# Optimization experiments

Measured on AMD Instinct MI355X. Metric: run time of the kernel, lower is better.

## Reference

```python
import jax, jax.numpy as jnp
import numpy as np

EPS = 1e-5
GROUPS = 8


def conv2d(x, w, b, pad):
    y = jax.lax.conv_general_dilated(
        x, w, window_strides=(1, 1), padding=[(pad, pad), (pad, pad)],
        dimension_numbers=('NCHW', 'OIHW', 'NCHW'))
    return y + b[None, :, None, None]


def setup_inputs() -> dict:
    key = jax.random.key(0)
    ks = jax.random.split(key, 8)
    b, c, h, w = 32, 256, 56, 56
    cg = c // GROUPS
    x = jax.random.normal(ks[0], (b, c, h, w), dtype=jnp.float32)
    w1 = jax.random.normal(ks[1], (cg, cg, 1, 1), dtype=jnp.float32) * 0.05
    b1 = jnp.zeros((cg,), dtype=jnp.float32)
    w3a = jax.random.normal(ks[2], (cg, cg, 3, 3), dtype=jnp.float32) * 0.05
    b3a = jnp.zeros((cg,), dtype=jnp.float32)
    w3b = jax.random.normal(ks[3], (c, c, 3, 3), dtype=jnp.float32) * 0.02
    b3b = jnp.zeros((c,), dtype=jnp.float32)
    gn_w = jnp.ones((cg,), dtype=jnp.float32)
    gn_b = jnp.zeros((cg,), dtype=jnp.float32)
    return {"x": x, "w1": w1, "b1": b1, "w3a": w3a, "b3a": b3a,
            "w3b": w3b, "b3b": b3b, "gn_w": gn_w, "gn_b": gn_b}


def reference(x, w1, b1, w3a, b3a, w3b, b3b, gn_w, gn_b):
    b, c, h, w = x.shape
    cg = c // GROUPS
    bg = b * GROUPS
    gx = x.reshape(bg, cg, h, w)

    # spatial attention on grouped channels
    x_h = gx.mean(axis=3, keepdims=True)                       # [bg,cg,h,1]
    x_w = gx.mean(axis=2, keepdims=True).transpose(0, 1, 3, 2)  # [bg,cg,w,1]
    hw = conv2d(jnp.concatenate([x_h, x_w], axis=2), w1, b1, 0)
    xh, xw = hw[:, :, :h], hw[:, :, h:]
    x0 = gx * jax.nn.sigmoid(xh) * jax.nn.sigmoid(xw.transpose(0, 1, 3, 2))

    # GroupNorm with num_groups == num_channels (per-channel over HxW)
    mu = x0.mean(axis=(2, 3), keepdims=True)
    var = x0.var(axis=(2, 3), keepdims=True)
    x1 = (x0 - mu) / jnp.sqrt(var + EPS) * gn_w[None, :, None, None] + gn_b[None, :, None, None]

    x2 = conv2d(gx, w3a, b3a, 1)

    # channel softmax-matmul attention (per group)
    x11 = jax.nn.softmax(x1.mean(axis=(2, 3)), axis=-1)[:, None, :]  # [bg,1,cg]
    x12 = x1.reshape(bg, cg, h * w)
    x21 = jax.nn.softmax(x2.mean(axis=(2, 3)), axis=-1)[:, None, :]
    x22 = x2.reshape(bg, cg, h * w)
    weights1 = (jnp.matmul(x11, x22) + jnp.matmul(x21, x12)).reshape(bg, 1, h, w)

    # BatchNorm2d(affine=False), batch statistics (training mode)
    xr = x0.reshape(b, c, h, w)
    bm = xr.mean(axis=(0, 2, 3), keepdims=True)
    bv = xr.var(axis=(0, 2, 3), keepdims=True)
    x3 = (xr - bm) / jnp.sqrt(bv + EPS)

    x4 = conv2d(x, w3b, b3b, 1)

    # spatial softmax-matmul attention over full channels
    x31 = jax.nn.softmax(x3.mean(axis=1).reshape(b, 1, h * w), axis=-1)  # [b,1,hw]
    x32 = x3.reshape(b, c, h * w).transpose(0, 2, 1)                     # [b,hw,c]
    x41 = jax.nn.softmax(x4.mean(axis=1).reshape(b, 1, h * w), axis=-1)
    x42 = x4.reshape(b, c, h * w).transpose(0, 2, 1)
    weights2 = (jnp.matmul(x31, x42) + jnp.matmul(x41, x32)).reshape(b, c, 1, 1)

    return (gx * jax.nn.sigmoid(weights1)).reshape(b, c, h, w) + x * jax.nn.sigmoid(weights2)
```

## Files before the change

kernel.cpp:

```cpp
#include <hip/hip_runtime.h>
#include <math.h>

#define B  32
#define C  256
#define HH 56
#define WW 56
#define HW 3136
#define G  8
#define CG 32
#define BG 256
#define GC 8192
#define EPSF 1e-5f

typedef __attribute__((ext_vector_type(8))) short short8;
typedef __attribute__((ext_vector_type(4))) float f32x4;

#define GLOAD16(g, l) __builtin_amdgcn_global_load_lds( \
    (const __attribute__((address_space(1))) void*)(g), \
    (__attribute__((address_space(3))) void*)(l), 16, 0, 0)

__device__ __forceinline__ float sigmoidf_(float v){ return 1.0f/(1.0f+__expf(-v)); }
__device__ __forceinline__ unsigned short f2bf(float v){
  unsigned u = __builtin_bit_cast(unsigned, v);
  u = u + 0x7FFFu + ((u>>16)&1u);
  return (unsigned short)(u>>16);
}
__device__ __forceinline__ float bf2f(unsigned short v){
  return __builtin_bit_cast(float, ((unsigned)v)<<16);
}

__global__ void kxt(const float* __restrict__ x, unsigned short* __restrict__ xt){
  int bid = blockIdx.x;
  int b = bid / 196; int r2 = bid % 196; int icb = r2 / 49; int pxb = r2 % 49;
  __shared__ float t[64][65];
  int tid = threadIdx.x;
  #pragma unroll
  for(int k=0;k<16;k++){
    int e = k*256 + tid;
    int ic = e>>6, px = e&63;
    t[ic][px] = x[((size_t)(b*256 + icb*64 + ic))*HW + pxb*64 + px];
  }
  __syncthreads();
  #pragma unroll
  for(int k=0;k<16;k++){
    int e = k*256 + tid;
    int px = e>>6, ic = e&63;
    int pxg = pxb*64 + px;
    int pi = pxg/56, pj = pxg%56;
    xt[(((size_t)b*58 + pi + 1)*58 + pj + 1)*256 + icb*64 + ic] = f2bf(t[ic][px]);
  }
}

__global__ void khalo(unsigned short* __restrict__ xt){
  int bid = blockIdx.x;
  int b = bid/228, hp = bid%228;
  int pi, pj;
  if(hp<58){pi=0;pj=hp;}
  else if(hp<116){pi=57;pj=hp-58;}
  else if(hp<172){pi=hp-116+1;pj=0;}
  else {pi=hp-172+1;pj=57;}
  xt[(((size_t)b*58+pi)*58+pj)*256 + threadIdx.x] = 0;
}

__global__ __launch_bounds__(256) void k1t(const unsigned short* __restrict__ xt,
    float* __restrict__ rowm, float* __restrict__ colm){
  int bid = blockIdx.x;
  int b = bid / 112; int r = bid % 112; int rc = r / 56; int idx = r % 56;
  int c = threadIdx.x;
  const unsigned short* xb = xt + (size_t)b*58*58*256 + c;
  float s = 0.f;
  if(rc == 0){
    #pragma unroll 8
    for(int j=0;j<56;j++) s += bf2f(xb[((size_t)(idx+1)*58 + (j+1))*256]);
    rowm[((size_t)b*256 + c)*56 + idx] = s*(1.0f/56.0f);
  } else {
    #pragma unroll 8
    for(int i=0;i<56;i++) s += bf2f(xb[((size_t)(i+1)*58 + (idx+1))*256]);
    colm[((size_t)b*256 + c)*56 + idx] = s*(1.0f/56.0f);
  }
}

__global__ void k2_hw(const float* __restrict__ rowm, const float* __restrict__ colm,
                      const float* __restrict__ w1, const float* __restrict__ b1,
                      float* __restrict__ sh, float* __restrict__ sw,
                      float* __restrict__ shT, float* __restrict__ swT){
  int bg = blockIdx.x;
  int b = bg>>3, g = bg&7;
  __shared__ float inb[32][112];
  __shared__ float wt[32*32];
  __shared__ float bb[32];
  for(int idx=threadIdx.x; idx<32*56; idx+=blockDim.x){
    int ic=idx/56, p=idx%56;
    inb[ic][p]    = rowm[(bg*32+ic)*56+p];
    inb[ic][56+p] = colm[(bg*32+ic)*56+p];
  }
  for(int idx=threadIdx.x; idx<1024; idx+=blockDim.x) wt[idx]=w1[idx];
  if(threadIdx.x<32) bb[threadIdx.x]=b1[threadIdx.x];
  __syncthreads();
  for(int o=threadIdx.x; o<32*112; o+=blockDim.x){
    int oc=o/112, p=o%112;
    float s=bb[oc];
    #pragma unroll
    for(int ic=0;ic<32;ic++) s += wt[oc*32+ic]*inb[ic][p];
    float sg = sigmoidf_(s);
    int c = g*32+oc;
    if(p<56){
      sh[(bg*32+oc)*56+p]=sg;
      shT[((size_t)b*56+p)*256 + c]=sg;
    } else {
      sw[(bg*32+oc)*56+(p-56)]=sg;
      swT[((size_t)b*56+(p-56))*256 + c]=sg;
    }
  }
}

__global__ void k2b_x11(const float* __restrict__ gnb, const float* __restrict__ b3a, float* __restrict__ x11){
  __shared__ float v[32];
  if(threadIdx.x<32) v[threadIdx.x]=gnb[threadIdx.x];
  __syncthreads();
  if(threadIdx.x==0){
    float m=-1e30f; for(int i=0;i<32;i++) m=fmaxf(m,v[i]);
    float s=0.f; for(int i=0;i<32;i++){ v[i]=__expf(v[i]-m); s+=v[i]; }
    float d=0.f;
    for(int i=0;i<32;i++){ float p=v[i]/s; x11[i]=p; d+=p*b3a[i]; }
    x11[32]=d;
  }
}

__global__ __launch_bounds__(256) void k3t(const unsigned short* __restrict__ xt,
    const float* __restrict__ shT, const float* __restrict__ swT,
    float* __restrict__ gsum, float* __restrict__ gsq){
  int bid = blockIdx.x;
  int b = bid / 56, i = bid % 56;
  int c = threadIdx.x;
  float shv = shT[((size_t)b*56+i)*256 + c];
  const unsigned short* xb = xt + ((size_t)(b*58 + i+1)*58 + 1)*256 + c;
  const float* swp = swT + (size_t)b*56*256 + c;
  float s=0.f, s2=0.f;
  #pragma unroll 8
  for(int j=0;j<56;j++){
    float x0 = bf2f(xb[(size_t)j*256]) * shv * swp[(size_t)j*256];
    s += x0; s2 += x0*x0;
  }
  atomicAdd(&gsum[b*256+c], s);
  atomicAdd(&gsq[b*256+c], s2);
}

__global__ void k4a(const float* __restrict__ gsum, const float* __restrict__ gsq,
                    float* __restrict__ mu, float* __restrict__ istd){
  int gc=blockIdx.x*256+threadIdx.x;
  float m=gsum[gc]*(1.0f/HW);
  float v=gsq[gc]*(1.0f/HW)-m*m;
  mu[gc]=m; istd[gc]=rsqrtf(v+EPSF);
}

__global__ void k4b(const float* __restrict__ gsum, const float* __restrict__ gsq,
                    float* __restrict__ bm, float* __restrict__ binv){
  int c=threadIdx.x;
  float s=0.f,s2=0.f;
  for(int b=0;b<B;b++){ s+=gsum[b*256+c]; s2+=gsq[b*256+c]; }
  float m=s*(1.0f/(B*HW));
  float v=s2*(1.0f/(B*HW))-m*m;
  bm[c]=m; binv[c]=rsqrtf(v+EPSF);
}

__global__ __launch_bounds__(128) void k5m(const unsigned short* __restrict__ xt,
    const unsigned short* __restrict__ wta, const float* __restrict__ x11,
    float* __restrict__ w1a, float* __restrict__ cs2){
  __shared__ short Bs[6*58*32];
  int bid = blockIdx.x;
  int xcd = bid & 7; int idx = bid >> 3;
  int b = xcd + 8*(idx/112); int idx2 = idx % 112;
  int g = idx2 / 14; int pt = idx2 % 14;
  int bg = b*8 + g;
  int i0 = pt*4;
  int tid = threadIdx.x;
  int lane = tid & 63, wv = tid >> 6;
  int q = lane >> 4, rl = lane & 15;
  const unsigned short* xb = xt + (size_t)b*58*58*256 + g*32;

  #pragma unroll
  for(int issue=0; issue<11; ++issue){
    int idxl = issue*128 + tid;
    if(idxl < 1392){
      int pl = idxl >> 2, ch = idxl & 3;
      int r = pl / 58, jj = pl - r*58;
      const unsigned short* src = xb + ((size_t)(i0 + r)*58 + jj)*256 + ((ch ^ ((pl>>1)&3))<<3);
      GLOAD16(src, &Bs[idxl*8]);
    }
  }
  __syncthreads();

  f32x4 acc[2][7];
  #pragma unroll
  for(int mi=0;mi<2;mi++)
    #pragma unroll
    for(int ni=0;ni<7;ni++) acc[mi][ni]=(f32x4){0.f,0.f,0.f,0.f};

  int pr[7], pj[7];
  #pragma unroll
  for(int ni=0;ni<7;ni++){
    int px = wv*112 + ni*16 + rl;
    pr[ni] = px/56; pj[ni] = px - pr[ni]*56;
  }

  for(int tap=0; tap<9; ++tap){
    int dy = tap/3, dx = tap - dy*3;
    short8 a[2], bfr[7];
    #pragma unroll
    for(int mi=0;mi<2;mi++)
      a[mi] = *(const short8*)(wta + tap*1024 + (mi*16+rl)*32 + q*8);
    #pragma unroll
    for(int ni=0;ni<7;ni++){
      int pix = (pr[ni] + dy)*58 + pj[ni] + dx;
      int cs = q ^ ((pix>>1)&3);
      bfr[ni] = *(const short8*)&Bs[pix*32 + cs*8];
    }
    #pragma unroll
    for(int mi=0;mi<2;mi++)
      #pragma unroll
      for(int ni=0;ni<7;ni++)
        acc[mi][ni] = __builtin_amdgcn_mfma_f32_16x16x32_bf16(a[mi], bfr[ni], acc[mi][ni], 0,0,0);
  }

  float x11v[2][4];
  #pragma unroll
  for(int mi=0;mi<2;mi++)
    #pragma unroll
    for(int r=0;r<4;r++) x11v[mi][r] = x11[mi*16 + q*4 + r];
  float x11b = x11[32];
  size_t pxg0 = (size_t)bg*HW + i0*56 + wv*112;
  #pragma unroll
  for(int ni=0;ni<7;ni++){
    float s=0.f;
    #pragma unroll
    for(int mi=0;mi<2;mi++)
      #pragma unroll
      for(int r=0;r<4;r++) s += x11v[mi][r]*acc[mi][ni][r];
    s += __shfl_xor(s,16,64);
    s += __shfl_xor(s,32,64);
    if(lane<16) w1a[pxg0 + ni*16 + lane] = s + x11b;
  }
  #pragma unroll
  for(int mi=0;mi<2;mi++){
    #pragma unroll
    for(int r=0;r<4;r++){
      float s=0.f;
      #pragma unroll
      for(int ni=0;ni<7;ni++) s += acc[mi][ni][r];
      s += __shfl_xor(s,1,64);
      s += __shfl_xor(s,2,64);
      s += __shfl_xor(s,4,64);
      s += __shfl_xor(s,8,64);
      if(rl==0) atomicAdd(&cs2[bg*32 + mi*16 + q*4 + r], s);
    }
  }
}

__global__ void k6(const float* __restrict__ cs2, const float* __restrict__ b3a,
                   const float* __restrict__ mu, const float* __restrict__ istd,
                   const float* __restrict__ gnw, const float* __restrict__ gnb,
                   float* __restrict__ av, float* __restrict__ cst){
  int bg=blockIdx.x; int t=threadIdx.x;
  float m = cs2[bg*32+t]*(1.0f/HW) + b3a[t];
  float mx=m;
  for(int off=16;off>0;off>>=1) mx=fmaxf(mx,__shfl_xor(mx,off,32));
  float e=__expf(m-mx);
  float s=e;
  for(int off=16;off>0;off>>=1) s+=__shfl_xor(s,off,32);
  float x21=e/s;
  int gc=bg*32+t;
  float is=istd[gc];
  av[gc]=x21*is*gnw[t];
  float cv=x21*(gnb[t]-mu[gc]*is*gnw[t]);
  for(int off=16;off>0;off>>=1) cv+=__shfl_xor(cv,off,32);
  if(t==0) cst[bg]=cv;
}

__global__ __launch_bounds__(256) void k7x(const unsigned short* __restrict__ xt,
    const float* __restrict__ shT, const float* __restrict__ swT,
    const float* __restrict__ av, const float* __restrict__ binv, const float* __restrict__ cst,
    const float* __restrict__ w1a, float* __restrict__ sg1, float* __restrict__ s3pre){
  int bid = blockIdx.x; int b = bid/56, i = bid%56;
  __shared__ float shs[256], avs[256], bins[256], cst8[8];
  int tid = threadIdx.x;
  shs[tid]  = shT[((size_t)b*56+i)*256 + tid];
  avs[tid]  = av[b*256 + tid];
  bins[tid] = binv[tid];
  if(tid<8) cst8[tid] = cst[b*8+tid];
  __syncthreads();
  int h = tid>>5, l = tid&31;
  int bg = l>>2;
  int c0 = l*8;
  float sh8[8], av8[8], bi8[8];
  #pragma unroll
  for(int m=0;m<8;m++){ sh8[m]=shs[c0+m]; av8[m]=avs[c0+m]; bi8[m]=bins[c0+m]; }
  float cstv = cst8[bg];
  for(int pass=0; pass<7; ++pass){
    int j = pass*8 + h;
    short8 xv = *(const short8*)(xt + (((size_t)b*58 + i+1)*58 + j+1)*256 + c0);
    const float* swp = swT + ((size_t)b*56 + j)*256 + c0;
    float ws=0.f, s3=0.f;
    #pragma unroll
    for(int m=0;m<8;m++){
      float x0 = bf2f((unsigned short)xv[m]) * sh8[m] * swp[m];
      ws += av8[m]*x0;
      s3 += bi8[m]*x0;
    }
    ws += __shfl_xor(ws,1,64);
    ws += __shfl_xor(ws,2,64);
    s3 += __shfl_xor(s3,1,64);
    s3 += __shfl_xor(s3,2,64);
    s3 += __shfl_xor(s3,4,64);
    s3 += __shfl_xor(s3,8,64);
    s3 += __shfl_xor(s3,16,64);
    int p = i*56 + j;
    if((l&3)==0){
      size_t o = ((size_t)(b*8+bg))*HW + p;
      sg1[o] = sigmoidf_(w1a[o] + ws + cstv);
    }
    if(l==0) s3pre[(size_t)b*HW + p] = s3*(1.0f/256.0f);
  }
}

__global__ void k_softmax_hw(const float* __restrict__ in, float* __restrict__ out, float scale){
  int b=blockIdx.x;
  const float* ip=in+(size_t)b*HW;
  float mx=-1e30f;
  for(int p=threadIdx.x;p<HW;p+=blockDim.x) mx=fmaxf(mx,ip[p]*scale);
  for(int off=32;off>0;off>>=1) mx=fmaxf(mx,__shfl_xor(mx,off,64));
  __shared__ float red[8];
  int wid=threadIdx.x>>6, lane=threadIdx.x&63;
  if(lane==0) red[wid]=mx;
  __syncthreads();
  mx=red[0];
  #pragma unroll
  for(int w=1;w<8;w++) mx=fmaxf(mx,red[w]);
  float s=0.f;
  for(int p=threadIdx.x;p<HW;p+=blockDim.x) s+=__expf(ip[p]*scale-mx);
  for(int off=32;off>0;off>>=1) s+=__shfl_down(s,off,64);
  __shared__ float red2[8];
  if(lane==0) red2[wid]=s;
  __syncthreads();
  s=red2[0];
  #pragma unroll
  for(int w=1;w<8;w++) s+=red2[w];
  float inv=1.0f/s;
  for(int p=threadIdx.x;p<HW;p+=blockDim.x) out[(size_t)b*HW+p]=__expf(ip[p]*scale-mx)*inv;
}

__global__ void kwt(const float* __restrict__ w3b, unsigned short* __restrict__ wt){
  int idx = blockIdx.x*256 + threadIdx.x;
  int tap = idx >> 16; int r = idx & 65535; int oc = r >> 8; int ic = r & 255;
  wt[idx] = f2bf(w3b[((size_t)oc*256 + ic)*9 + tap]);
}

__global__ void kwta(const float* __restrict__ w3a, unsigned short* __restrict__ wta){
  int idx = blockIdx.x*256 + threadIdx.x;
  if(idx < 9216){
    int tap = idx >> 10; int r = idx & 1023; int oc = r >> 5; int ic = r & 31;
    wta[idx] = f2bf(w3a[((size_t)oc*32 + ic)*9 + tap]);
  }
}

__global__ __launch_bounds__(512) void k9m(const unsigned short* __restrict__ xt,
    const unsigned short* __restrict__ wt, const float* __restrict__ x31,
    float* __restrict__ s4pre, float* __restrict__ w2a){
  __shared__ short Ab[2][128*32];
  __shared__ short Bb[2][224*32];
  int bid = blockIdx.x;
  int xcd = bid & 7; int idx = bid >> 3;
  int b = xcd + 8*(idx/28); int rr = idx % 28;
  int pt = rr >> 1; int oct = rr & 1;
  int i0 = pt*4; int ocb = oct*128;
  int tid = threadIdx.x;
  int lane = tid & 63, wv = tid >> 6;
  int wm = wv & 3, wn = wv >> 2;
  int q = lane >> 4, rl = lane & 15;
  const unsigned short* xb = xt + (size_t)b*58*58*256;

  #define STAGE_A(BUF, TAP, IC0) do{ \
    int idxl = tid; int oc_ = idxl>>2, cs_ = idxl&3; \
    const unsigned short* src = wt + (((size_t)(TAP)*256 + ocb + oc_)*256 + (IC0) + (((cs_ ^ ((oc_>>1)&3)))<<3)); \
    GLOAD16(src, &Ab[BUF][idxl*8]); }while(0)
  #define STAGE_B(BUF, TAP, IC0) do{ \
    int dy_ = (TAP)/3, dx_ = (TAP)%3; \
    { int idxl = tid; int px_ = idxl>>2, cs_ = idxl&3; int r_ = px_/56, j_ = px_ - r_*56; \
      const unsigned short* src = xb + ((size_t)((i0 + r_ + dy_)*58 + (j_ + dx_)))*256 + (IC0) + ((cs_ ^ ((px_>>1)&3))<<3); \
      GLOAD16(src, &Bb[BUF][idxl*8]); } \
    if(tid < 384){ int idxl = tid + 512; int px_ = idxl>>2, cs_ = idxl&3; int r_ = px_/56, j_ = px_ - r_*56; \
      const unsigned short* src = xb + ((size_t)((i0 + r_ + dy_)*58 + (j_ + dx_)))*256 + (IC0) + ((cs_ ^ ((px_>>1)&3))<<3); \
      GLOAD16(src, &Bb[BUF][idxl*8]); } }while(0)

  STAGE_A(0, 0, 0);
  STAGE_B(0, 0, 0);
  __syncthreads();

  f32x4 acc[2][7];
  #pragma unroll
  for(int mi=0;mi<2;mi++)
    #pragma unroll
    for(int ni=0;ni<7;ni++) acc[mi][ni] = (f32x4){0.f,0.f,0.f,0.f};

  for(int t=0; t<72; ++t){
    int cur = t & 1;
    if(t+1 < 72){
      int tn = t+1; int tap = tn >> 3; int ic0 = (tn & 7) << 5;
      STAGE_A(cur^1, tap, ic0);
      STAGE_B(cur^1, tap, ic0);
    }
    short8 a[2], bf[7];
    #pragma unroll
    for(int mi=0;mi<2;mi++){
      int row = wm*32 + mi*16 + rl;
      int cs = q ^ ((row>>1)&3);
      a[mi] = *(const short8*)&Ab[cur][row*32 + cs*8];
    }
    #pragma unroll
    for(int ni=0;ni<7;ni++){
      int px = wn*112 + ni*16 + rl;
      int cs = q ^ ((px>>1)&3);
      bf[ni] = *(const short8*)&Bb[cur][px*32 + cs*8];
    }
    #pragma unroll
    for(int mi=0;mi<2;mi++)
      #pragma unroll
      for(int ni=0;ni<7;ni++)
        acc[mi][ni] = __builtin_amdgcn_mfma_f32_16x16x32_bf16(a[mi], bf[ni], acc[mi][ni], 0,0,0);
    __syncthreads();
  }
  #undef STAGE_A
  #undef STAGE_B

  size_t pxbase = (size_t)b*HW + i0*56 + wn*112;
  #pragma unroll
  for(int ni=0;ni<7;ni++){
    float s = 0.f;
    #pragma unroll
    for(int mi=0;mi<2;mi++){
      s += acc[mi][ni][0]+acc[mi][ni][1]+acc[mi][ni][2]+acc[mi][ni][3];
    }
    s += __shfl_xor(s, 16, 64);
    s += __shfl_xor(s, 32, 64);
    if(lane < 16) atomicAdd(&s4pre[pxbase + ni*16 + lane], s);
  }
  float x31v[7];
  #pragma unroll
  for(int ni=0;ni<7;ni++) x31v[ni] = x31[pxbase + ni*16 + rl];
  #pragma unroll
  for(int mi=0;mi<2;mi++){
    #pragma unroll
    for(int r=0;r<4;r++){
      float s = 0.f;
      #pragma unroll
      for(int ni=0;ni<7;ni++) s += x31v[ni]*acc[mi][ni][r];
      s += __shfl_xor(s, 1, 64);
      s += __shfl_xor(s, 2, 64);
      s += __shfl_xor(s, 4, 64);
      s += __shfl_xor(s, 8, 64);
      if(rl == 0) atomicAdd(&w2a[b*256 + ocb + wm*32 + mi*16 + q*4 + r], s);
    }
  }
}

__global__ __launch_bounds__(256) void k11f(const float* __restrict__ x, const float* __restrict__ sh,
    const float* __restrict__ sw, const float* __restrict__ x41, const float* __restrict__ bm,
    const float* __restrict__ binv, const float* __restrict__ w2a, const float* __restrict__ b3b,
    const float* __restrict__ sg1, float* __restrict__ out){
  int gc=blockIdx.x; int b=gc>>8, c=gc&255, bg=gc>>5;
  __shared__ float xs[HW];
  __shared__ float ssh[56], ssw[56];
  __shared__ float red[4];
  int tid=threadIdx.x;
  if(tid<56) ssh[tid]=sh[gc*56+tid];
  else if(tid>=64&&tid<120) ssw[tid-64]=sw[gc*56+tid-64];
  const float* xp=x+(size_t)gc*HW;
  const float* wp=x41+(size_t)b*HW;
  for(int p=tid;p<HW;p+=256) xs[p]=xp[p];
  __syncthreads();
  float s=0.f;
  for(int p=tid;p<HW;p+=256){
    float x0=xs[p]*ssh[p/56]*ssw[p%56];
    s+=wp[p]*x0;
  }
  for(int off=32;off>0;off>>=1) s+=__shfl_down(s,off,64);
  int wid=tid>>6, lane=tid&63;
  if(lane==0) red[wid]=s;
  __syncthreads();
  float t=red[0]+red[1]+red[2]+red[3];
  float sg2=sigmoidf_(w2a[gc]+b3b[c]+binv[c]*t-bm[c]*binv[c]);
  const float* sp=sg1+(size_t)bg*HW;
  float* op=out+(size_t)gc*HW;
  for(int p=tid;p<HW;p+=256){
    op[p]=xs[p]*(sp[p]+sg2);
  }
}

extern "C" void kernel_launch(void* const* d_in, const int* in_sizes, int n_in,
                              void* d_out, int out_size, void* d_ws, size_t ws_size,
                              hipStream_t stream) {
  const float* x   = (const float*)d_in[0];
  const float* w1  = (const float*)d_in[1];
  const float* b1  = (const float*)d_in[2];
  const float* w3a = (const float*)d_in[3];
  const float* b3a = (const float*)d_in[4];
  const float* w3b = (const float*)d_in[5];
  const float* b3b = (const float*)d_in[6];
  const float* gnw = (const float*)d_in[7];
  const float* gnb = (const float*)d_in[8];
  float* out=(float*)d_out;
  float* ws=(float*)d_ws;

  float* rowm=ws;
  float* colm=rowm+458752;
  float* sh  =colm+458752;
  float* sw  =sh+458752;
  float* x11 =sw+458752;
  float* gsum=x11+64;
  float* gsq =gsum+8192;
  float* mu  =gsq+8192;
  float* istd=mu+8192;
  float* bm  =istd+8192;
  float* binv=bm+256;
  float* cs2 =binv+256;
  float* w1a =cs2+8192;
  float* av  =w1a+802816;
  float* cst =av+8192;
  float* s3  =cst+256;
  float* x31 =s3+100352;
  float* s4  =x31+100352;
  float* x41 =s4+100352;
  float* w2a =x41+100352;
  float* shT =w2a+8192;
  float* swT =shT+458752;
  float* sg1 =swT+458752;
  unsigned short* xt = (unsigned short*)(sg1 + 802816);
  unsigned short* wtb = xt + (size_t)32*58*58*256;
  unsigned short* wta = wtb + 589824;

  kxt<<<32*4*49,256,0,stream>>>(x, xt);
  khalo<<<32*228,256,0,stream>>>(xt);
  kwt<<<2304,256,0,stream>>>(w3b, wtb);
  kwta<<<36,256,0,stream>>>(w3a, wta);

  k1t<<<32*112,256,0,stream>>>(xt,rowm,colm);
  k2_hw<<<BG,128,0,stream>>>(rowm,colm,w1,b1,sh,sw,shT,swT);
  k2b_x11<<<1,32,0,stream>>>(gnb,b3a,x11);
  hipMemsetAsync(gsum,0,2*8192*sizeof(float),stream);
  k3t<<<32*56,256,0,stream>>>(xt,shT,swT,gsum,gsq);
  k4a<<<32,256,0,stream>>>(gsum,gsq,mu,istd);
  k4b<<<1,256,0,stream>>>(gsum,gsq,bm,binv);
  hipMemsetAsync(cs2,0,8192*sizeof(float),stream);
  k5m<<<256*14,128,0,stream>>>(xt,wta,x11,w1a,cs2);
  k6<<<BG,32,0,stream>>>(cs2,b3a,mu,istd,gnw,gnb,av,cst);
  k7x<<<B*56,256,0,stream>>>(xt,shT,swT,av,binv,cst,w1a,sg1,s3);
  k_softmax_hw<<<B,512,0,stream>>>(s3,x31,1.0f);
  hipMemsetAsync(w2a,0,8192*sizeof(float),stream);
  hipMemsetAsync(s4,0,(size_t)HW*B*sizeof(float),stream);
  k9m<<<32*28,512,0,stream>>>(xt,wtb,x31,s4,w2a);
  k_softmax_hw<<<B,512,0,stream>>>(s4,x41,1.0f/256.0f);
  k11f<<<GC,256,0,stream>>>(x,sh,sw,x41,bm,binv,w2a,b3b,sg1,out);
}
```

Measured before the change: 351.7 us.

## Triple-buffer conv3x3 MFMA mainloop with vmcnt-based partial waits

Changes the k9m implicit-GEMM conv loop from double to triple buffering in LDS, prefetching three K-steps ahead. Instead of a full __syncthreads after each step (which drains all outstanding loads), it uses explicit s_waitcnt vmcnt with per-thread counts so only the oldest stage must land. The aim is to hide global-to-LDS load latency behind MFMA work. The cost is more LDS per block (about 74KB), which may lower occupancy, plus fragile hand-counted wait values.

```diff
diff --git a/kernel.cpp b/kernel.cpp
--- a/kernel.cpp
+++ b/kernel.cpp
@@ -366,8 +366,8 @@
 __global__ __launch_bounds__(512) void k9m(const unsigned short* __restrict__ xt,
     const unsigned short* __restrict__ wt, const float* __restrict__ x31,
     float* __restrict__ s4pre, float* __restrict__ w2a){
-  __shared__ short Ab[2][128*32];
-  __shared__ short Bb[2][224*32];
+  __shared__ short Ab[3][128*32];
+  __shared__ short Bb[3][224*32];
   int bid = blockIdx.x;
   int xcd = bid & 7; int idx = bid >> 3;
   int b = xcd + 8*(idx/28); int rr = idx % 28;
@@ -379,22 +379,22 @@
   int q = lane >> 4, rl = lane & 15;
   const unsigned short* xb = xt + (size_t)b*58*58*256;
 
-  #define STAGE_A(BUF, TAP, IC0) do{ \
-    int idxl = tid; int oc_ = idxl>>2, cs_ = idxl&3; \
-    const unsigned short* src = wt + (((size_t)(TAP)*256 + ocb + oc_)*256 + (IC0) + (((cs_ ^ ((oc_>>1)&3)))<<3)); \
-    GLOAD16(src, &Ab[BUF][idxl*8]); }while(0)
-  #define STAGE_B(BUF, TAP, IC0) do{ \
-    int dy_ = (TAP)/3, dx_ = (TAP)%3; \
+  #define STAGE(BUF, T) do{ \
+    int tap_ = (T) >> 3; int ic0_ = ((T) & 7) << 5; \
+    { int idxl = tid; int oc_ = idxl>>2, cs_ = idxl&3; \
+      const unsigned short* src = wt + (((size_t)tap_*256 + ocb + oc_)*256 + ic0_ + (((cs_ ^ ((oc_>>1)&3)))<<3)); \
+      GLOAD16(src, &Ab[BUF][idxl*8]); } \
+    int dy_ = tap_/3, dx_ = tap_%3; \
     { int idxl = tid; int px_ = idxl>>2, cs_ = idxl&3; int r_ = px_/56, j_ = px_ - r_*56; \
-      const unsigned short* src = xb + ((size_t)((i0 + r_ + dy_)*58 + (j_ + dx_)))*256 + (IC0) + ((cs_ ^ ((px_>>1)&3))<<3); \
+      const unsigned short* src = xb + ((size_t)((i0 + r_ + dy_)*58 + (j_ + dx_)))*256 + ic0_ + ((cs_ ^ ((px_>>1)&3))<<3); \
       GLOAD16(src, &Bb[BUF][idxl*8]); } \
     if(tid < 384){ int idxl = tid + 512; int px_ = idxl>>2, cs_ = idxl&3; int r_ = px_/56, j_ = px_ - r_*56; \
-      const unsigned short* src = xb + ((size_t)((i0 + r_ + dy_)*58 + (j_ + dx_)))*256 + (IC0) + ((cs_ ^ ((px_>>1)&3))<<3); \
+      const unsigned short* src = xb + ((size_t)((i0 + r_ + dy_)*58 + (j_ + dx_)))*256 + ic0_ + ((cs_ ^ ((px_>>1)&3))<<3); \
       GLOAD16(src, &Bb[BUF][idxl*8]); } }while(0)
 
-  STAGE_A(0, 0, 0);
-  STAGE_B(0, 0, 0);
-  __syncthreads();
+  STAGE(0, 0);
+  STAGE(1, 1);
+  STAGE(2, 2);
 
   f32x4 acc[2][7];
   #pragma unroll
@@ -402,13 +402,19 @@
     #pragma unroll
     for(int ni=0;ni<7;ni++) acc[mi][ni] = (f32x4){0.f,0.f,0.f,0.f};
 
+  int cur = 0;
   for(int t=0; t<72; ++t){
-    int cur = t & 1;
-    if(t+1 < 72){
-      int tn = t+1; int tap = tn >> 3; int ic0 = (tn & 7) << 5;
-      STAGE_A(cur^1, tap, ic0);
-      STAGE_B(cur^1, tap, ic0);
-    }
+    if(t <= 69){
+      if(tid < 384) asm volatile("s_waitcnt vmcnt(6)" ::: "memory");
+      else          asm volatile("s_waitcnt vmcnt(4)" ::: "memory");
+    } else if(t == 70){
+      if(tid < 384) asm volatile("s_waitcnt vmcnt(3)" ::: "memory");
+      else          asm volatile("s_waitcnt vmcnt(2)" ::: "memory");
+    } else {
+      asm volatile("s_waitcnt vmcnt(0)" ::: "memory");
+    }
+    __builtin_amdgcn_s_barrier();
+    __builtin_amdgcn_sched_barrier(0);
     short8 a[2], bf[7];
     #pragma unroll
     for(int mi=0;mi<2;mi++){
@@ -427,10 +433,12 @@
       #pragma unroll
       for(int ni=0;ni<7;ni++)
         acc[mi][ni] = __builtin_amdgcn_mfma_f32_16x16x32_bf16(a[mi], bf[ni], acc[mi][ni], 0,0,0);
-    __syncthreads();
-  }
-  #undef STAGE_A
-  #undef STAGE_B
+    __builtin_amdgcn_sched_barrier(0);
+    __builtin_amdgcn_s_barrier();
+    if(t+3 < 72) STAGE(cur, t+3);
+    cur = (cur==2) ? 0 : cur+1;
+  }
+  #undef STAGE
 
   size_t pxbase = (size_t)b*HW + i0*56 + wn*112;
   #pragma unroll
```

Result: no change. 353.4 us (+0.5%).
